# Kernel optimization log

Hardware: AMD Instinct MI355X
Metric: run time of the kernel (lower is better)

## Reference

```python
import jax, jax.numpy as jnp
import numpy as np

B, N, D = 4, 2048, 512      # batch, seq, dim_in
DK = DV = 512               # dim_k == dim_v (required by fc input width)
NH = 8
HK = DK // NH               # per-head dk == dv == 64
SCALE = 1.0 / np.sqrt(HK)
LN_EPS = 1e-5


def setup_inputs() -> dict:
    key = jax.random.key(0)
    ks = jax.random.split(key, 8)
    s = 0.02
    return {
        "x": jax.random.normal(ks[0], (B, N, D), dtype=jnp.float32),
        "Wq": jax.random.normal(ks[1], (D, DK), dtype=jnp.float32) * s,
        "Wk": jax.random.normal(ks[2], (D, DK), dtype=jnp.float32) * s,
        "Wv": jax.random.normal(ks[3], (D, DV), dtype=jnp.float32) * s,
        "Wf": jax.random.normal(ks[4], (2 * DK, D), dtype=jnp.float32) * s,
        "bf": jnp.zeros((D,), dtype=jnp.float32),
        "gamma": jnp.ones((D,), dtype=jnp.float32),
        "beta": jnp.zeros((D,), dtype=jnp.float32),
    }


def reference(x, Wq, Wk, Wv, Wf, bf, gamma, beta):
    b, n, _ = x.shape
    # projections -> [b, nh, n, hk]; q_c/q_f etc. are identical in the source,
    # so compute once.
    def proj(W):
        return jnp.einsum('bnd,dk->bnk', x, W).reshape(b, n, NH, -1).transpose(0, 2, 1, 3)
    q, k, v = proj(Wq), proj(Wk), proj(Wv)

    # conventional branch: softmax over n x n scores
    dist_c = jax.nn.softmax(jnp.einsum('bhqd,bhkd->bhqk', q, k) * SCALE, axis=-1)
    att_c = jnp.einsum('bhqk,bhkd->bhqd', dist_c, v)          # [b,nh,n,hk]
    att_c = att_c.transpose(0, 2, 1, 3).reshape(b, n, DV)

    # feature branch: softmax over dk x dk scores (linear-complexity variant)
    dist_f = jax.nn.softmax(jnp.einsum('bhnk,bhnq->bhkq', k, q) * SCALE, axis=-1)
    att_f = jnp.einsum('bhnd,bhdq->bhnq', v, dist_f)           # [b,nh,n,hk]
    att_f = att_f.transpose(0, 2, 1, 3).reshape(b, n, DV)

    att = jnp.concatenate([att_c, att_f], axis=2)              # [b,n,2*dk]
    out = jax.nn.relu(att @ Wf + bf)                           # dropout=eval (identity)
    out = out + x
    mu = jnp.mean(out, axis=-1, keepdims=True)
    var = jnp.var(out, axis=-1, keepdims=True)
    out = (out - mu) * jax.lax.rsqrt(var + LN_EPS) * gamma + beta
    return out
```

## Files before the change

### kernel.cpp

```cpp
#include <hip/hip_runtime.h>
#include <math.h>
#include <stdint.h>

#define B_   4
#define N_   2048
#define D_   512
#define DK_  512
#define NH_  8
#define HK_  64
#define LN_EPS_ 1e-5f
#define QS_  0.18033688011112042f

typedef unsigned short u16;
typedef __attribute__((ext_vector_type(8))) short short8;
typedef __attribute__((ext_vector_type(4))) float f32x4;
typedef __attribute__((ext_vector_type(8))) unsigned short u16x8;

__device__ __forceinline__ u16 f2bf(float x) {
    uint32_t u = __builtin_bit_cast(uint32_t, x);
    return (u16)((u + 0x7fffu + ((u >> 16) & 1u)) >> 16);
}
__device__ __forceinline__ u16 f2bf_fast(float x) {
    return (u16)((__builtin_bit_cast(uint32_t, x) + 0x8000u) >> 16);
}
__device__ __forceinline__ uint32_t pack2bf(float a, float b) {
    return (uint32_t)f2bf_fast(a) | ((uint32_t)f2bf_fast(b) << 16);
}
__device__ __forceinline__ float exp2f_fast(float x) {
    return __builtin_amdgcn_exp2f(x);
}

__device__ __forceinline__ void gload16(const void* g, void* l) {
    __builtin_amdgcn_global_load_lds(
        reinterpret_cast<const __attribute__((address_space(1))) void*>(
            reinterpret_cast<uintptr_t>(g)),
        reinterpret_cast<__attribute__((address_space(3))) void*>(
            static_cast<uint32_t>(reinterpret_cast<uintptr_t>(l))),
        16, 0, 0);
}

__global__ __launch_bounds__(256) void conv_bf16_kernel(
    const float* __restrict__ src, u16* __restrict__ dst, int n)
{
    const int i = (blockIdx.x * 256 + threadIdx.x) * 8;
    if (i >= n) return;
    const float4 a = *reinterpret_cast<const float4*>(&src[i]);
    const float4 b = *reinterpret_cast<const float4*>(&src[i + 4]);
    u16x8 o;
    o[0] = f2bf(a.x); o[1] = f2bf(a.y); o[2] = f2bf(a.z); o[3] = f2bf(a.w);
    o[4] = f2bf(b.x); o[5] = f2bf(b.y); o[6] = f2bf(b.z); o[7] = f2bf(b.w);
    *reinterpret_cast<u16x8*>(&dst[i]) = o;
}

__global__ __launch_bounds__(256) void tc3_kernel(
    const float* __restrict__ W0, const float* __restrict__ W1,
    const float* __restrict__ W2, u16* __restrict__ Wt)
{
    __shared__ float t[32][33];
    const float* W = blockIdx.z == 0 ? W0 : (blockIdx.z == 1 ? W1 : W2);
    u16* dst = Wt + (size_t)blockIdx.z * 512 * 512;
    const int tid = threadIdx.x;
    const int kt = blockIdx.y * 32, nt = blockIdx.x * 32;
    {
        const int r = tid >> 3, c0 = (tid & 7) * 4;
        const float4 v = *reinterpret_cast<const float4*>(
            &W[(size_t)(kt + r) * 512 + nt + c0]);
        t[r][c0] = v.x; t[r][c0 + 1] = v.y; t[r][c0 + 2] = v.z; t[r][c0 + 3] = v.w;
    }
    __syncthreads();
    {
        const int nidx = tid >> 3, kc = (tid & 7) * 4;
        u16 o[4];
        #pragma unroll
        for (int j = 0; j < 4; ++j) o[j] = f2bf(t[kc + j][nidx]);
        *reinterpret_cast<ushort4*>(&dst[(size_t)(nt + nidx) * 512 + kt + kc]) =
            make_ushort4(o[0], o[1], o[2], o[3]);
    }
}

__global__ __launch_bounds__(256) void tcf_kernel(
    const float* __restrict__ W, u16* __restrict__ Wt)
{
    __shared__ float t[32][33];
    const int tid = threadIdx.x;
    const int kt = blockIdx.y * 32, nt = blockIdx.x * 32;
    {
        const int r = tid >> 3, c0 = (tid & 7) * 4;
        const float4 v = *reinterpret_cast<const float4*>(
            &W[(size_t)(kt + r) * 512 + nt + c0]);
        t[r][c0] = v.x; t[r][c0 + 1] = v.y; t[r][c0 + 2] = v.z; t[r][c0 + 3] = v.w;
    }
    __syncthreads();
    {
        const int nidx = tid >> 3, kc = (tid & 7) * 4;
        u16 o[4];
        #pragma unroll
        for (int j = 0; j < 4; ++j) o[j] = f2bf(t[kc + j][nidx]);
        *reinterpret_cast<ushort4*>(&Wt[(size_t)(nt + nidx) * 1024 + kt + kc]) =
            make_ushort4(o[0], o[1], o[2], o[3]);
    }
}

template<int BM, int BN, int MODE>
__global__ __launch_bounds__(256) void gemm_bf16(
    const u16* __restrict__ A, const u16* __restrict__ Bt,
    float* __restrict__ Cf, u16* __restrict__ qb, u16* __restrict__ kb,
    u16* __restrict__ vb, u16* __restrict__ vt, int M, int Nc, int K,
    const float* __restrict__ bias, const float* __restrict__ resid)
{
    constexpr int MI = BM / 32, NI = BN / 32;
    constexpr int AL = BM / 32, BL = BN / 32;
    __shared__ u16 As[BM * 64];
    __shared__ u16 Bs[BN * 64];
    const int tid = threadIdx.x;
    const int lane = tid & 63, wave = tid >> 6;
    const int wm = wave >> 1, wn = wave & 1;
    const int l15 = lane & 15, lg = lane >> 4;

    const int nwg = gridDim.x;
    const int bid = ((int)blockIdx.x & 7) * (nwg >> 3) + ((int)blockIdx.x >> 3);
    const int ntiles = Nc / BN;
    const int nt = (bid % ntiles) * BN;
    const int mt = (bid / ntiles) * BM;

    f32x4 acc[MI][NI] = {};

    for (int kt = 0; kt < K; kt += 64) {
        __syncthreads();
        #pragma unroll
        for (int i = 0; i < AL; ++i) {
            const int ob = (wave * AL + i) * 1024;
            const int o = ob + lane * 16;
            const int row = o >> 7;
            const int inner = (o & 127) ^ ((row & 7) << 4);
            gload16((const char*)A + ((size_t)(mt + row) * K + kt) * 2 + inner,
                    (char*)As + ob);
        }
        #pragma unroll
        for (int i = 0; i < BL; ++i) {
            const int ob = (wave * BL + i) * 1024;
            const int o = ob + lane * 16;
            const int row = o >> 7;
            const int inner = (o & 127) ^ ((row & 7) << 4);
            gload16((const char*)Bt + ((size_t)(nt + row) * K + kt) * 2 + inner,
                    (char*)Bs + ob);
        }
        __syncthreads();
        #pragma unroll
        for (int ks = 0; ks < 2; ++ks) {
            const int kb2 = ks * 32 + lg * 8;
            short8 af[MI], bfr[NI];
            #pragma unroll
            for (int mi = 0; mi < MI; ++mi) {
                const int r = wm * (BM / 2) + mi * 16 + l15;
                af[mi] = *reinterpret_cast<const short8*>(
                    &As[r * 64 + (kb2 ^ ((r & 7) << 3))]);
            }
            #pragma unroll
            for (int ni = 0; ni < NI; ++ni) {
                const int r = wn * (BN / 2) + ni * 16 + l15;
                bfr[ni] = *reinterpret_cast<const short8*>(
                    &Bs[r * 64 + (kb2 ^ ((r & 7) << 3))]);
            }
            #pragma unroll
            for (int mi = 0; mi < MI; ++mi)
                #pragma unroll
                for (int ni = 0; ni < NI; ++ni)
                    acc[mi][ni] = __builtin_amdgcn_mfma_f32_16x16x32_bf16(
                        af[mi], bfr[ni], acc[mi][ni], 0, 0, 0);
        }
    }

    #pragma unroll
    for (int mi = 0; mi < MI; ++mi) {
        #pragma unroll
        for (int ni = 0; ni < NI; ++ni) {
            const int col = nt + wn * (BN / 2) + ni * 16 + l15;
            const int row0 = mt + wm * (BM / 2) + mi * 16 + lg * 4;
            if (MODE == 1) {
                if (col < 512) {
                    #pragma unroll
                    for (int jj = 0; jj < 4; ++jj)
                        qb[(size_t)(row0 + jj) * 512 + col] =
                            f2bf(acc[mi][ni][jj] * QS_);
                } else if (col < 1024) {
                    #pragma unroll
                    for (int jj = 0; jj < 4; ++jj)
                        kb[(size_t)(row0 + jj) * 512 + col - 512] =
                            f2bf(acc[mi][ni][jj]);
                } else {
                    const int dfull = col - 1024;
                    const int hh = dfull >> 6, dd = dfull & 63;
                    const int bb = row0 >> 11, nn = row0 & 2047;
                    u16 o4[4];
                    #pragma unroll
                    for (int jj = 0; jj < 4; ++jj) {
                        o4[jj] = f2bf(acc[mi][ni][jj]);
                        vb[(size_t)(row0 + jj) * 512 + dfull] = o4[jj];
                    }
                    *reinterpret_cast<ushort4*>(
                        &vt[(((size_t)(bb * NH_ + hh)) * HK_ + dd) * N_ + nn]) =
                        make_ushort4(o4[0], o4[1], o4[2], o4[3]);
                }
            } else {
                #pragma unroll
                for (int jj = 0; jj < 4; ++jj) {
                    const size_t row = (size_t)(row0 + jj);
                    float v = acc[mi][ni][jj];
                    v += bias[col];
                    v = fmaxf(v, 0.0f);
                    v += resid[row * Nc + col];
                    Cf[row * Nc + col] = v;
                }
            }
        }
    }
}

__global__ __launch_bounds__(256) void flash_bf16_kernel(
    const u16* __restrict__ Qb, const u16* __restrict__ Kb,
    const u16* __restrict__ Vt, u16* __restrict__ att)
{
    __shared__ u16 Ks0[64 * 64];
    __shared__ u16 Ks1[64 * 64];
    __shared__ u16 Vs0[64 * 64];
    __shared__ u16 Vs1[64 * 64];
    __shared__ u16 Ps[128 * 64];
    const int tid = threadIdx.x;
    const int lane = tid & 63, wave = tid >> 6;
    const int l15 = lane & 15, lg = lane >> 4;
    const int lbid = (((int)blockIdx.x & 7) << 6) + ((int)blockIdx.x >> 3);
    const int qt = lbid & 15, h = (lbid >> 4) & 7, b = lbid >> 7;

    short8 aq[2][2];
    #pragma unroll
    for (int qs = 0; qs < 2; ++qs) {
        const int qrow = qt * 128 + qs * 64 + wave * 16 + l15;
        const u16* qp = Qb + ((size_t)(b * N_ + qrow)) * DK_ + h * HK_ + lg * 8;
        aq[qs][0] = *reinterpret_cast<const short8*>(qp);
        aq[qs][1] = *reinterpret_cast<const short8*>(qp + 32);
    }
    short8 ones;
    #pragma unroll
    for (int i = 0; i < 8; ++i) ones[i] = (short)0x3F80;

    const u16* Kbase = Kb + (size_t)b * N_ * DK_ + (size_t)h * HK_;
    const u16* Vbase = Vt + ((size_t)(b * NH_ + h)) * HK_ * N_;
    unsigned long long* Ps64 = reinterpret_cast<unsigned long long*>(Ps);

    f32x4 o[2][5] = {};
    float m_[2] = {-1e30f, -1e30f};

#define STAGE(ktile, KBUF, VBUF) do {                                          \
    _Pragma("unroll")                                                          \
    for (int i_ = 0; i_ < 2; ++i_) {                                           \
        const int ob_ = (wave * 2 + i_) * 1024;                                \
        const int oo_ = ob_ + lane * 16;                                       \
        const int row_ = oo_ >> 7;                                             \
        const int inner_ = (oo_ & 127) ^ ((row_ & 7) << 4);                    \
        gload16((const char*)Kbase +                                           \
                    ((size_t)((ktile) * 64 + row_) * DK_) * 2 + inner_,        \
                (char*)(KBUF) + ob_);                                          \
        gload16((const char*)Vbase +                                           \
                    ((size_t)row_ * N_ + (ktile) * 64) * 2 + inner_,           \
                (char*)(VBUF) + ob_);                                          \
    }                                                                          \
} while (0)

#define FLASH_STEP(KBUF, VBUF) do {                                            \
    f32x4 s[2][4] = {};                                                        \
    __builtin_amdgcn_s_setprio(1);                                             \
    _Pragma("unroll")                                                          \
    for (int ks = 0; ks < 2; ++ks) {                                           \
        const int kb2 = ks * 32 + lg * 8;                                      \
        _Pragma("unroll")                                                      \
        for (int t = 0; t < 4; ++t) {                                          \
            const int r = t * 16 + l15;                                        \
            const short8 bk = *reinterpret_cast<const short8*>(                \
                &(KBUF)[r * 64 + (kb2 ^ ((r & 7) << 3))]);                     \
            s[0][t] = __builtin_amdgcn_mfma_f32_16x16x32_bf16(                 \
                bk, aq[0][ks], s[0][t], 0, 0, 0);                              \
            s[1][t] = __builtin_amdgcn_mfma_f32_16x16x32_bf16(                 \
                bk, aq[1][ks], s[1][t], 0, 0, 0);                              \
        }                                                                      \
    }                                                                          \
    __builtin_amdgcn_s_setprio(0);                                             \
    float rmax[2], cm;                                                         \
    _Pragma("unroll")                                                          \
    for (int qs = 0; qs < 2; ++qs) {                                           \
        float a0 = fmaxf(fmaxf(s[qs][0][0], s[qs][0][1]),                      \
                         fmaxf(s[qs][0][2], s[qs][0][3]));                     \
        float a1 = fmaxf(fmaxf(s[qs][1][0], s[qs][1][1]),                      \
                         fmaxf(s[qs][1][2], s[qs][1][3]));                     \
        float a2 = fmaxf(fmaxf(s[qs][2][0], s[qs][2][1]),                      \
                         fmaxf(s[qs][2][2], s[qs][2][3]));                     \
        float a3 = fmaxf(fmaxf(s[qs][3][0], s[qs][3][1]),                      \
                         fmaxf(s[qs][3][2], s[qs][3][3]));                     \
        rmax[qs] = fmaxf(fmaxf(a0, a1), fmaxf(a2, a3));                        \
    }                                                                          \
    cm = fmaxf(rmax[0] - m_[0], rmax[1] - m_[1]);                              \
    if (__any(cm > 8.0f)) {                                                    \
        _Pragma("unroll")                                                      \
        for (int qs = 0; qs < 2; ++qs) {                                       \
            float rm = rmax[qs];                                               \
            rm = fmaxf(rm, __shfl_xor(rm, 16));                                \
            rm = fmaxf(rm, __shfl_xor(rm, 32));                                \
            const float newm = fmaxf(m_[qs], rm);                              \
            const float fac = exp2f_fast(m_[qs] - newm);                       \
            m_[qs] = newm;                                                     \
            float facq[4];                                                     \
            _Pragma("unroll")                                                  \
            for (int jj = 0; jj < 4; ++jj)                                     \
                facq[jj] = __shfl(fac, lg * 4 + jj);                           \
            _Pragma("unroll")                                                  \
            for (int t = 0; t < 5; ++t)                                        \
                _Pragma("unroll")                                              \
                for (int jj = 0; jj < 4; ++jj)                                 \
                    o[qs][t][jj] *= facq[jj];                                  \
        }                                                                      \
    }                                                                          \
    _Pragma("unroll")                                                          \
    for (int qs = 0; qs < 2; ++qs) {                                           \
        const int prow = qs * 64 + wave * 16 + l15;                            \
        const int pb64 = prow * 16;                                            \
        const int sw1 = (prow & 7) << 1;                                       \
        _Pragma("unroll")                                                      \
        for (int t = 0; t < 4; ++t) {                                          \
            const float p0 = exp2f_fast(s[qs][t][0] - m_[qs]);                 \
            const float p1 = exp2f_fast(s[qs][t][1] - m_[qs]);                 \
            const float p2 = exp2f_fast(s[qs][t][2] - m_[qs]);                 \
            const float p3 = exp2f_fast(s[qs][t][3] - m_[qs]);                 \
            const uint32_t lo = pack2bf(p0, p1);                               \
            const uint32_t hi = pack2bf(p2, p3);                               \
            Ps64[pb64 + ((t * 4 + lg) ^ sw1)] =                                \
                (unsigned long long)lo | ((unsigned long long)hi << 32);       \
        }                                                                      \
    }                                                                          \
    __builtin_amdgcn_s_setprio(1);                                             \
    _Pragma("unroll")                                                          \
    for (int ks = 0; ks < 2; ++ks) {                                           \
        const int kb2 = ks * 32 + lg * 8;                                      \
        const int pr0 = wave * 16 + l15;                                       \
        const int pr1 = 64 + pr0;                                              \
        const short8 ap0 = *reinterpret_cast<const short8*>(                   \
            &Ps[pr0 * 64 + (kb2 ^ ((pr0 & 7) << 3))]);                         \
        const short8 ap1 = *reinterpret_cast<const short8*>(                   \
            &Ps[pr1 * 64 + (kb2 ^ ((pr1 & 7) << 3))]);                         \
        _Pragma("unroll")                                                      \
        for (int t = 0; t < 4; ++t) {                                          \
            const int dr = t * 16 + l15;                                       \
            const short8 bv = *reinterpret_cast<const short8*>(                \
                &(VBUF)[dr * 64 + (kb2 ^ ((dr & 7) << 3))]);                   \
            o[0][t] = __builtin_amdgcn_mfma_f32_16x16x32_bf16(                 \
                ap0, bv, o[0][t], 0, 0, 0);                                    \
            o[1][t] = __builtin_amdgcn_mfma_f32_16x16x32_bf16(                 \
                ap1, bv, o[1][t], 0, 0, 0);                                    \
        }                                                                      \
        o[0][4] = __builtin_amdgcn_mfma_f32_16x16x32_bf16(                     \
            ap0, ones, o[0][4], 0, 0, 0);                                      \
        o[1][4] = __builtin_amdgcn_mfma_f32_16x16x32_bf16(                     \
            ap1, ones, o[1][4], 0, 0, 0);                                      \
    }                                                                          \
    __builtin_amdgcn_s_setprio(0);                                             \
} while (0)

    STAGE(0, Ks0, Vs0);
    __syncthreads();

    #pragma unroll 1
    for (int kt = 0; kt < N_ / 64; kt += 2) {
        STAGE(kt + 1, Ks1, Vs1);
        FLASH_STEP(Ks0, Vs0);
        __syncthreads();
        if (kt + 2 < N_ / 64) STAGE(kt + 2, Ks0, Vs0);
        FLASH_STEP(Ks1, Vs1);
        __syncthreads();
    }
#undef STAGE
#undef FLASH_STEP

    #pragma unroll
    for (int qs = 0; qs < 2; ++qs)
        #pragma unroll
        for (int jj = 0; jj < 4; ++jj) {
            const float inv = 1.0f / o[qs][4][jj];
            const size_t row = (size_t)b * N_ + qt * 128 + qs * 64 + wave * 16 + lg * 4 + jj;
            #pragma unroll
            for (int t = 0; t < 4; ++t)
                att[row * (2 * DK_) + h * HK_ + t * 16 + l15] =
                    f2bf_fast(o[qs][t][jj] * inv);
        }
}

__global__ __launch_bounds__(256) void featS_mfma(
    const u16* __restrict__ Kb, const u16* __restrict__ Qb,
    float* __restrict__ partials)
{
    __shared__ u16 KsT[64 * 64];
    __shared__ u16 QsT[64 * 64];
    const int tid = threadIdx.x;
    const int lane = tid & 63, wave = tid >> 6;
    const int l15 = lane & 15, lg = lane >> 4;
    const int ns = blockIdx.x, h = blockIdx.y, b = blockIdx.z;
    const size_t hbase = (size_t)b * N_ * DK_ + (size_t)h * HK_;

    f32x4 acc[4] = {};
    for (int c = 0; c < 4; ++c) {
        const int n0 = ns * 256 + c * 64;
        __syncthreads();
        #pragma unroll
        for (int it = 0; it < 2; ++it) {
            const int idx = tid + it * 256;
            const int n = idx >> 3, d0 = (idx & 7) * 8;
            const u16x8 kv = *reinterpret_cast<const u16x8*>(
                &Kb[hbase + (size_t)(n0 + n) * DK_ + d0]);
            const u16x8 qv = *reinterpret_cast<const u16x8*>(
                &Qb[hbase + (size_t)(n0 + n) * DK_ + d0]);
            #pragma unroll
            for (int j = 0; j < 8; ++j) {
                const int r = d0 + j;
                const int cidx = n ^ ((r & 7) << 3);
                KsT[r * 64 + cidx] = kv[j];
                QsT[r * 64 + cidx] = qv[j];
            }
        }
        __syncthreads();
        #pragma unroll
        for (int ks = 0; ks < 2; ++ks) {
            const int kb2 = ks * 32 + lg * 8;
            const int ar = wave * 16 + l15;
            const short8 aK = *reinterpret_cast<const short8*>(
                &KsT[ar * 64 + (kb2 ^ ((ar & 7) << 3))]);
            #pragma unroll
            for (int ni = 0; ni < 4; ++ni) {
                const int br = ni * 16 + l15;
                const short8 bQ = *reinterpret_cast<const short8*>(
                    &QsT[br * 64 + (kb2 ^ ((br & 7) << 3))]);
                acc[ni] = __builtin_amdgcn_mfma_f32_16x16x32_bf16(aK, bQ, acc[ni], 0, 0, 0);
            }
        }
    }
    const int bh = b * NH_ + h;
    #pragma unroll
    for (int ni = 0; ni < 4; ++ni)
        #pragma unroll
        for (int jj = 0; jj < 4; ++jj) {
            const int row = wave * 16 + lg * 4 + jj;
            partials[(((size_t)ns * 32 + bh) * 64 + row) * 64 + ni * 16 + l15] =
                acc[ni][jj];
        }
}

__global__ __launch_bounds__(256) void featSM_kernel(
    const float* __restrict__ partials, u16* __restrict__ distfT)
{
    const int bh = blockIdx.x, tid = threadIdx.x;
    const int r = tid >> 2, qq = tid & 3;
    float v[16];
    #pragma unroll
    for (int j = 0; j < 16; ++j) v[j] = 0.0f;
    for (int s = 0; s < 8; ++s) {
        const float4* pp = reinterpret_cast<const float4*>(
            &partials[(((size_t)s * 32 + bh) * 64 + r) * 64 + qq * 16]);
        #pragma unroll
        for (int j4 = 0; j4 < 4; ++j4) {
            const float4 a = pp[j4];
            v[j4 * 4 + 0] += a.x; v[j4 * 4 + 1] += a.y;
            v[j4 * 4 + 2] += a.z; v[j4 * 4 + 3] += a.w;
        }
    }
    float m = v[0];
    #pragma unroll
    for (int j = 1; j < 16; ++j) m = fmaxf(m, v[j]);
    m = fmaxf(m, __shfl_xor(m, 1));
    m = fmaxf(m, __shfl_xor(m, 2));
    float sum = 0.0f;
    #pragma unroll
    for (int j = 0; j < 16; ++j) { v[j] = exp2f_fast(v[j] - m); sum += v[j]; }
    sum += __shfl_xor(sum, 1);
    sum += __shfl_xor(sum, 2);
    const float inv = 1.0f / sum;
    #pragma unroll
    for (int j = 0; j < 16; ++j)
        distfT[(size_t)bh * 4096 + (qq * 16 + j) * 64 + r] = f2bf_fast(v[j] * inv);
}

__global__ __launch_bounds__(256) void featAV_mfma(
    const u16* __restrict__ V, const u16* __restrict__ distfT,
    u16* __restrict__ att)
{
    __shared__ u16 Bs[64 * 64];
    __shared__ u16 As[64 * 64];
    const int tid = threadIdx.x;
    const int lane = tid & 63, wave = tid >> 6;
    const int l15 = lane & 15, lg = lane >> 4;
    const int ns = blockIdx.x, h = blockIdx.y, b = blockIdx.z;
    const int bh = b * NH_ + h;

    #pragma unroll
    for (int it = 0; it < 2; ++it) {
        const int idx = tid + it * 256;
        const int r = idx >> 3, c0 = (idx & 7) * 8;
        const u16x8 dv = *reinterpret_cast<const u16x8*>(
            &distfT[(size_t)bh * 4096 + r * 64 + c0]);
        *reinterpret_cast<u16x8*>(&Bs[r * 64 + (c0 ^ ((r & 7) << 3))]) = dv;
    }

    for (int c = 0; c < 4; ++c) {
        const int n0 = ns * 256 + c * 64;
        __syncthreads();
        #pragma unroll
        for (int i = 0; i < 2; ++i) {
            const int ob = (wave * 2 + i) * 1024;
            const int o_ = ob + lane * 16;
            const int row = o_ >> 7;
            const int inner = (o_ & 127) ^ ((row & 7) << 4);
            gload16((const char*)V + ((size_t)(b * N_ + n0 + row) * DK_ + h * HK_) * 2 + inner,
                    (char*)As + ob);
        }
        __syncthreads();
        f32x4 acc[4] = {};
        #pragma unroll
        for (int ks = 0; ks < 2; ++ks) {
            const int kb2 = ks * 32 + lg * 8;
            const int ar = wave * 16 + l15;
            const short8 av = *reinterpret_cast<const short8*>(
                &As[ar * 64 + (kb2 ^ ((ar & 7) << 3))]);
            #pragma unroll
            for (int ni = 0; ni < 4; ++ni) {
                const int br = ni * 16 + l15;
                const short8 bd = *reinterpret_cast<const short8*>(
                    &Bs[br * 64 + (kb2 ^ ((br & 7) << 3))]);
                acc[ni] = __builtin_amdgcn_mfma_f32_16x16x32_bf16(av, bd, acc[ni], 0, 0, 0);
            }
        }
        #pragma unroll
        for (int ni = 0; ni < 4; ++ni)
            #pragma unroll
            for (int jj = 0; jj < 4; ++jj)
                att[((size_t)b * N_ + n0 + wave * 16 + lg * 4 + jj) * (2 * DK_)
                    + 512 + h * HK_ + ni * 16 + l15] = f2bf_fast(acc[ni][jj]);
    }
}

__global__ __launch_bounds__(256) void ln_kernel(
    const float* __restrict__ fc, const float* __restrict__ gamma,
    const float* __restrict__ beta, float* __restrict__ out)
{
    __shared__ float red[8];
    const int row = blockIdx.x, tid = threadIdx.x;
    const int c = tid * 2;
    const float2 v = *reinterpret_cast<const float2*>(&fc[(size_t)row * D_ + c]);
    float s = v.x + v.y;
    float sq = v.x * v.x + v.y * v.y;
    #pragma unroll
    for (int off = 32; off >= 1; off >>= 1) {
        s  += __shfl_xor(s, off);
        sq += __shfl_xor(sq, off);
    }
    const int lane = tid & 63, w = tid >> 6;
    if (lane == 0) { red[w] = s; red[4 + w] = sq; }
    __syncthreads();
    s  = red[0] + red[1] + red[2] + red[3];
    sq = red[4] + red[5] + red[6] + red[7];
    const float mu = s * (1.0f / D_);
    const float var = sq * (1.0f / D_) - mu * mu;
    const float rstd = rsqrtf(var + LN_EPS_);
    float2 o;
    o.x = (v.x - mu) * rstd * gamma[c] + beta[c];
    o.y = (v.y - mu) * rstd * gamma[c + 1] + beta[c + 1];
    *reinterpret_cast<float2*>(&out[(size_t)row * D_ + c]) = o;
}

extern "C" void kernel_launch(void* const* d_in, const int* in_sizes, int n_in,
                              void* d_out, int out_size, void* d_ws, size_t ws_size,
                              hipStream_t stream)
{
    (void)in_sizes; (void)n_in; (void)out_size; (void)ws_size;
    const float* x     = (const float*)d_in[0];
    const float* Wq    = (const float*)d_in[1];
    const float* Wk    = (const float*)d_in[2];
    const float* Wv    = (const float*)d_in[3];
    const float* Wf    = (const float*)d_in[4];
    const float* bf    = (const float*)d_in[5];
    const float* gamma = (const float*)d_in[6];
    const float* beta  = (const float*)d_in[7];
    float* out = (float*)d_out;

    char* w = (char*)d_ws;
    const size_t SZE = (size_t)B_ * N_ * DK_;
    u16* xb     = (u16*)w;   w += SZE * 2;
    u16* wqkvT  = (u16*)w;   w += (size_t)1536 * 512 * 2;
    u16* wfT    = (u16*)w;   w += (size_t)512 * 1024 * 2;
    u16* qb     = (u16*)w;   w += SZE * 2;
    u16* kb     = (u16*)w;   w += SZE * 2;
    u16* vb     = (u16*)w;   w += SZE * 2;
    u16* vt     = (u16*)w;   w += SZE * 2;
    u16* attb   = (u16*)w;   w += SZE * 2 * 2;
    float* partials = (float*)w; w += (size_t)8 * 32 * 4096 * 4;
    u16* distfT = (u16*)w;   w += (size_t)32 * 4096 * 2;
    float* fcout = (float*)w;

    const dim3 blk(256);
    const int M = B_ * N_;

    conv_bf16_kernel<<<dim3((B_ * N_ * D_) / 2048), blk, 0, stream>>>(x, xb, B_ * N_ * D_);
    tc3_kernel<<<dim3(16, 16, 3), blk, 0, stream>>>(Wq, Wk, Wv, wqkvT);
    tcf_kernel<<<dim3(16, 32), blk, 0, stream>>>(Wf, wfT);

    gemm_bf16<128, 128, 1><<<dim3(768), blk, 0, stream>>>(
        xb, wqkvT, nullptr, qb, kb, vb, vt, M, 1536, 512, nullptr, nullptr);

    flash_bf16_kernel<<<dim3(512), blk, 0, stream>>>(qb, kb, vt, attb);

    featS_mfma<<<dim3(8, NH_, B_), blk, 0, stream>>>(kb, qb, partials);
    featSM_kernel<<<dim3(32), blk, 0, stream>>>(partials, distfT);
    featAV_mfma<<<dim3(8, NH_, B_), blk, 0, stream>>>(vb, distfT, attb);

    gemm_bf16<64, 128, 2><<<dim3(512), blk, 0, stream>>>(
        attb, wfT, fcout, nullptr, nullptr, nullptr, nullptr, M, D_, 2 * DK_, bf, x);

    ln_kernel<<<dim3(M), blk, 0, stream>>>(fcout, gamma, beta, out);
}
```

Measured before the change: 143.1 us.

## Merge prep kernels, store fc output as bf16, use hardware bf16 pack

Merges the x conversion and the three weight transpose kernels into one prep kernel, which saves launches. The fc GEMM epilogue now writes its pre-LayerNorm output as bf16 instead of fp32, and LayerNorm reads it back as bf16. This halves the intermediate traffic but rounds the residual sum before normalisation. The flash kernel packs P into bf16 with the v_cvt_pk_bf16_f32 instruction instead of manual bit arithmetic.

After: 134.4 us. 1.06x faster.

```diff
diff --git a/kernel.cpp b/kernel.cpp
--- a/kernel.cpp
+++ b/kernel.cpp
@@ -23,8 +23,13 @@
 __device__ __forceinline__ u16 f2bf_fast(float x) {
     return (u16)((__builtin_bit_cast(uint32_t, x) + 0x8000u) >> 16);
 }
-__device__ __forceinline__ uint32_t pack2bf(float a, float b) {
-    return (uint32_t)f2bf_fast(a) | ((uint32_t)f2bf_fast(b) << 16);
+__device__ __forceinline__ float b2f(u16 v) {
+    return __builtin_bit_cast(float, (uint32_t)v << 16);
+}
+__device__ __forceinline__ uint32_t cvtpk_bf16(float lo, float hi) {
+    uint32_t r;
+    asm("v_cvt_pk_bf16_f32 %0, %1, %2" : "=v"(r) : "v"(lo), "v"(hi));
+    return r;
 }
 __device__ __forceinline__ float exp2f_fast(float x) {
     return __builtin_amdgcn_exp2f(x);
@@ -39,32 +44,42 @@
         16, 0, 0);
 }
 
-__global__ __launch_bounds__(256) void conv_bf16_kernel(
-    const float* __restrict__ src, u16* __restrict__ dst, int n)
-{
-    const int i = (blockIdx.x * 256 + threadIdx.x) * 8;
-    if (i >= n) return;
-    const float4 a = *reinterpret_cast<const float4*>(&src[i]);
-    const float4 b = *reinterpret_cast<const float4*>(&src[i + 4]);
-    u16x8 o;
-    o[0] = f2bf(a.x); o[1] = f2bf(a.y); o[2] = f2bf(a.z); o[3] = f2bf(a.w);
-    o[4] = f2bf(b.x); o[5] = f2bf(b.y); o[6] = f2bf(b.z); o[7] = f2bf(b.w);
-    *reinterpret_cast<u16x8*>(&dst[i]) = o;
-}
-
-__global__ __launch_bounds__(256) void tc3_kernel(
-    const float* __restrict__ W0, const float* __restrict__ W1,
-    const float* __restrict__ W2, u16* __restrict__ Wt)
+__global__ __launch_bounds__(256) void prep_kernel(
+    const float* __restrict__ x, const float* __restrict__ Wq,
+    const float* __restrict__ Wk, const float* __restrict__ Wv,
+    const float* __restrict__ Wf, u16* __restrict__ xb,
+    u16* __restrict__ wqkvT, u16* __restrict__ wfT)
 {
     __shared__ float t[32][33];
-    const float* W = blockIdx.z == 0 ? W0 : (blockIdx.z == 1 ? W1 : W2);
-    u16* dst = Wt + (size_t)blockIdx.z * 512 * 512;
-    const int tid = threadIdx.x;
-    const int kt = blockIdx.y * 32, nt = blockIdx.x * 32;
+    const int bid = blockIdx.x, tid = threadIdx.x;
+    if (bid < 2048) {
+        const int i = (bid * 256 + tid) * 8;
+        const float4 a = *reinterpret_cast<const float4*>(&x[i]);
+        const float4 b = *reinterpret_cast<const float4*>(&x[i + 4]);
+        u16x8 o;
+        o[0] = f2bf(a.x); o[1] = f2bf(a.y); o[2] = f2bf(a.z); o[3] = f2bf(a.w);
+        o[4] = f2bf(b.x); o[5] = f2bf(b.y); o[6] = f2bf(b.z); o[7] = f2bf(b.w);
+        *reinterpret_cast<u16x8*>(&xb[i]) = o;
+        return;
+    }
+    const float* W;
+    u16* dst;
+    int K, Nc, nt, kt;
+    if (bid < 2816) {
+        const int z = (bid - 2048) >> 8, rem = (bid - 2048) & 255;
+        W = z == 0 ? Wq : (z == 1 ? Wk : Wv);
+        dst = wqkvT + (size_t)z * 512 * 512;
+        K = 512; Nc = 512;
+        nt = (rem & 15) * 32; kt = (rem >> 4) * 32;
+    } else {
+        const int rem = bid - 2816;
+        W = Wf; dst = wfT; K = 1024; Nc = 512;
+        nt = (rem & 15) * 32; kt = (rem >> 4) * 32;
+    }
     {
         const int r = tid >> 3, c0 = (tid & 7) * 4;
         const float4 v = *reinterpret_cast<const float4*>(
-            &W[(size_t)(kt + r) * 512 + nt + c0]);
+            &W[(size_t)(kt + r) * Nc + nt + c0]);
         t[r][c0] = v.x; t[r][c0 + 1] = v.y; t[r][c0 + 2] = v.z; t[r][c0 + 3] = v.w;
     }
     __syncthreads();
@@ -73,30 +88,7 @@
         u16 o[4];
         #pragma unroll
         for (int j = 0; j < 4; ++j) o[j] = f2bf(t[kc + j][nidx]);
-        *reinterpret_cast<ushort4*>(&dst[(size_t)(nt + nidx) * 512 + kt + kc]) =
-            make_ushort4(o[0], o[1], o[2], o[3]);
-    }
-}
-
-__global__ __launch_bounds__(256) void tcf_kernel(
-    const float* __restrict__ W, u16* __restrict__ Wt)
-{
-    __shared__ float t[32][33];
-    const int tid = threadIdx.x;
-    const int kt = blockIdx.y * 32, nt = blockIdx.x * 32;
-    {
-        const int r = tid >> 3, c0 = (tid & 7) * 4;
-        const float4 v = *reinterpret_cast<const float4*>(
-            &W[(size_t)(kt + r) * 512 + nt + c0]);
-        t[r][c0] = v.x; t[r][c0 + 1] = v.y; t[r][c0 + 2] = v.z; t[r][c0 + 3] = v.w;
-    }
-    __syncthreads();
-    {
-        const int nidx = tid >> 3, kc = (tid & 7) * 4;
-        u16 o[4];
-        #pragma unroll
-        for (int j = 0; j < 4; ++j) o[j] = f2bf(t[kc + j][nidx]);
-        *reinterpret_cast<ushort4*>(&Wt[(size_t)(nt + nidx) * 1024 + kt + kc]) =
+        *reinterpret_cast<ushort4*>(&dst[(size_t)(nt + nidx) * K + kt + kc]) =
             make_ushort4(o[0], o[1], o[2], o[3]);
     }
 }
@@ -104,7 +96,7 @@
 template<int BM, int BN, int MODE>
 __global__ __launch_bounds__(256) void gemm_bf16(
     const u16* __restrict__ A, const u16* __restrict__ Bt,
-    float* __restrict__ Cf, u16* __restrict__ qb, u16* __restrict__ kb,
+    u16* __restrict__ qb, u16* __restrict__ kb,
     u16* __restrict__ vb, u16* __restrict__ vt, int M, int Nc, int K,
     const float* __restrict__ bias, const float* __restrict__ resid)
 {
@@ -210,7 +202,7 @@
                     v += bias[col];
                     v = fmaxf(v, 0.0f);
                     v += resid[row * Nc + col];
-                    Cf[row * Nc + col] = v;
+                    qb[row * Nc + col] = f2bf(v);
                 }
             }
         }
@@ -330,8 +322,8 @@
             const float p1 = exp2f_fast(s[qs][t][1] - m_[qs]);                 \
             const float p2 = exp2f_fast(s[qs][t][2] - m_[qs]);                 \
             const float p3 = exp2f_fast(s[qs][t][3] - m_[qs]);                 \
-            const uint32_t lo = pack2bf(p0, p1);                               \
-            const uint32_t hi = pack2bf(p2, p3);                               \
+            const uint32_t lo = cvtpk_bf16(p0, p1);                            \
+            const uint32_t hi = cvtpk_bf16(p2, p3);                            \
             Ps64[pb64 + ((t * 4 + lg) ^ sw1)] =                                \
                 (unsigned long long)lo | ((unsigned long long)hi << 32);       \
         }                                                                      \
@@ -544,15 +536,17 @@
 }
 
 __global__ __launch_bounds__(256) void ln_kernel(
-    const float* __restrict__ fc, const float* __restrict__ gamma,
+    const u16* __restrict__ fc, const float* __restrict__ gamma,
     const float* __restrict__ beta, float* __restrict__ out)
 {
     __shared__ float red[8];
     const int row = blockIdx.x, tid = threadIdx.x;
     const int c = tid * 2;
-    const float2 v = *reinterpret_cast<const float2*>(&fc[(size_t)row * D_ + c]);
-    float s = v.x + v.y;
-    float sq = v.x * v.x + v.y * v.y;
+    const uint32_t pv = *reinterpret_cast<const uint32_t*>(&fc[(size_t)row * D_ + c]);
+    const float vx = b2f((u16)(pv & 0xffffu));
+    const float vy = b2f((u16)(pv >> 16));
+    float s = vx + vy;
+    float sq = vx * vx + vy * vy;
     #pragma unroll
     for (int off = 32; off >= 1; off >>= 1) {
         s  += __shfl_xor(s, off);
@@ -567,8 +561,8 @@
     const float var = sq * (1.0f / D_) - mu * mu;
     const float rstd = rsqrtf(var + LN_EPS_);
     float2 o;
-    o.x = (v.x - mu) * rstd * gamma[c] + beta[c];
-    o.y = (v.y - mu) * rstd * gamma[c + 1] + beta[c + 1];
+    o.x = (vx - mu) * rstd * gamma[c] + beta[c];
+    o.y = (vy - mu) * rstd * gamma[c + 1] + beta[c + 1];
     *reinterpret_cast<float2*>(&out[(size_t)row * D_ + c]) = o;
 }
 
@@ -599,17 +593,15 @@
     u16* attb   = (u16*)w;   w += SZE * 2 * 2;
     float* partials = (float*)w; w += (size_t)8 * 32 * 4096 * 4;
     u16* distfT = (u16*)w;   w += (size_t)32 * 4096 * 2;
-    float* fcout = (float*)w;
+    u16* fcout  = (u16*)w;
 
     const dim3 blk(256);
     const int M = B_ * N_;
 
-    conv_bf16_kernel<<<dim3((B_ * N_ * D_) / 2048), blk, 0, stream>>>(x, xb, B_ * N_ * D_);
-    tc3_kernel<<<dim3(16, 16, 3), blk, 0, stream>>>(Wq, Wk, Wv, wqkvT);
-    tcf_kernel<<<dim3(16, 32), blk, 0, stream>>>(Wf, wfT);
+    prep_kernel<<<dim3(3328), blk, 0, stream>>>(x, Wq, Wk, Wv, Wf, xb, wqkvT, wfT);
 
     gemm_bf16<128, 128, 1><<<dim3(768), blk, 0, stream>>>(
-        xb, wqkvT, nullptr, qb, kb, vb, vt, M, 1536, 512, nullptr, nullptr);
+        xb, wqkvT, qb, kb, vb, vt, M, 1536, 512, nullptr, nullptr);
 
     flash_bf16_kernel<<<dim3(512), blk, 0, stream>>>(qb, kb, vt, attb);
 
@@ -618,7 +610,7 @@
     featAV_mfma<<<dim3(8, NH_, B_), blk, 0, stream>>>(vb, distfT, attb);
 
     gemm_bf16<64, 128, 2><<<dim3(512), blk, 0, stream>>>(
-        attb, wfT, fcout, nullptr, nullptr, nullptr, nullptr, M, D_, 2 * DK_, bf, x);
+        attb, wfT, fcout, nullptr, nullptr, nullptr, M, D_, 2 * DK_, bf, x);
 
     ln_kernel<<<dim3(M), blk, 0, stream>>>(fcout, gamma, beta, out);
 }
```
